# Kernel tuning notes

Measured on AMD Instinct MI355X. Metric: run time of the kernel, lower is better.

Reference implementation:

```python
import jax, jax.numpy as jnp
import numpy as np

B, T, F = 4096, 256, 20
VOCAB, EMB = 1281, 4
UNITS = (64, 32, 32, 32)


def setup_inputs() -> dict:
    key = jax.random.key(0)
    ks = jax.random.split(key, 16)
    feats = jax.random.normal(ks[0], (B, T, F), jnp.float32)
    ids = jax.random.randint(ks[1], (B, T), 0, VOCAB).astype(jnp.float32)
    input_tensor = feats.at[:, :, 1].set(ids)  # column 1 = org ids
    W_emb = jax.random.normal(ks[2], (VOCAB, EMB), jnp.float32) * 0.1
    in_dims = (F - 2 + 1 + EMB,) + UNITS[:-1]  # (23, 64, 32, 32)
    out = {"input_tensor": input_tensor, "W_emb": W_emb}
    for i, (din, u) in enumerate(zip(in_dims, UNITS)):
        out[f"k{i}"] = jax.random.normal(ks[3 + 3 * i], (din, 3 * u), jnp.float32) * 0.1
        out[f"rk{i}"] = jax.random.normal(ks[4 + 3 * i], (u, 3 * u), jnp.float32) * 0.1
        out[f"b{i}"] = jnp.zeros((2, 3 * u), jnp.float32)  # [input_bias, recurrent_bias] (reset_after)
    out["Wd"] = jax.random.normal(ks[15], (UNITS[-1], 2), jnp.float32) * 0.1
    out["bd"] = jnp.zeros((2,), jnp.float32)
    return out


def _gru(h, x, k, rk, b):
    # Keras GRUCell, reset_after=True (TF2 default)
    mx = x @ k + b[0]
    mh = h @ rk + b[1]
    xz, xr, xh = jnp.split(mx, 3, axis=-1)
    hz, hr, hh = jnp.split(mh, 3, axis=-1)
    z = jax.nn.sigmoid(xz + hz)
    r = jax.nn.sigmoid(xr + hr)
    hc = jnp.tanh(xh + r * hh)
    return z * h + (1.0 - z) * hc


def reference(input_tensor, W_emb, k0, rk0, b0, k1, rk1, b1, k2, rk2, b2, k3, rk3, b3, Wd, bd):
    f0 = input_tensor[:, :, :1]                      # [B,T,1]
    ids = input_tensor[:, :, 1].astype(jnp.int32)    # [B,T]
    rest = input_tensor[:, :, 2:]                    # [B,T,F-2]
    emb = W_emb[ids]                                 # [B,T,EMB]
    x = jnp.concatenate([f0, rest, emb], axis=-1)    # [B,T,F+3]
    xs = jnp.swapaxes(x, 0, 1)                       # [T,B,F+3]
    bsz = x.shape[0]
    h_init = tuple(jnp.zeros((bsz, u), x.dtype) for u in UNITS)
    layer_params = ((k0, rk0, b0), (k1, rk1, b1), (k2, rk2, b2), (k3, rk3, b3))

    def step(carry, xt):
        hs = []
        inp = xt
        for h, (k, rk, b) in zip(carry, layer_params):
            h = _gru(h, inp, k, rk, b)
            hs.append(h)
            inp = h
        return tuple(hs), None

    hs, _ = jax.lax.scan(step, h_init, xs)
    # return_sequences + [:, -1, :] == final hidden state of last layer
    logits = hs[-1] @ Wd + bd
    return jax.nn.softmax(logits, axis=-1)
```

## Files before the change

### kernel.cpp

```cpp
#include <hip/hip_runtime.h>


typedef __attribute__((ext_vector_type(8))) __bf16 bf16x8;
typedef __attribute__((ext_vector_type(4))) float f32x4;

#define TT 256
#define FF 20
#define BT 16
#define CH 64
#define SH0 72
#define SH1 40
#define XSTR 648
#define NTHR 768

__device__ __forceinline__ f32x4 mfma16(bf16x8 a, bf16x8 b, f32x4 c) {
  return __builtin_amdgcn_mfma_f32_16x16x32_bf16(a, b, c, 0, 0, 0);
}

__device__ __forceinline__ float sigm(float x) {
  return __builtin_amdgcn_rcpf(1.f + __builtin_amdgcn_exp2f(-1.44269504f * x));
}
__device__ __forceinline__ float tanh_(float x) {
  return __builtin_amdgcn_rcpf(1.f + __builtin_amdgcn_exp2f(-2.88539008f * x)) * 2.f - 1.f;
}

__device__ __forceinline__ bf16x8 bfragW(const float* W, int Kreal, int N,
                                         int ncol, int kbase) {
  bf16x8 r;
#pragma unroll
  for (int j = 0; j < 8; ++j) {
    int k = kbase + j;
    r[j] = (__bf16)(k < Kreal ? W[k * N + ncol] : 0.f);
  }
  return r;
}

extern "C" __global__ void __launch_bounds__(NTHR, 3)
gru4(const float* __restrict__ inp, const float* __restrict__ Wemb,
     const float* __restrict__ k0, const float* __restrict__ rk0, const float* __restrict__ b0,
     const float* __restrict__ k1, const float* __restrict__ rk1, const float* __restrict__ b1,
     const float* __restrict__ k2, const float* __restrict__ rk2, const float* __restrict__ b2,
     const float* __restrict__ k3, const float* __restrict__ rk3, const float* __restrict__ b3,
     const float* __restrict__ Wd, const float* __restrict__ bd,
     float* __restrict__ out)
{
  __shared__ __align__(16) __bf16 x_ch[CH * XSTR];
  __shared__ __align__(16) __bf16 h0_lds[2][BT * SH0];
  __shared__ __align__(16) __bf16 h1_lds[2][BT * SH1];
  __shared__ __align__(16) __bf16 h2_lds[2][BT * SH1];
  __shared__ __align__(16) __bf16 h3_lds[2][BT * SH1];
  __shared__ __align__(16) float h3f[BT * 32];

  const int tid  = threadIdx.x;
  const int lane = tid & 63;
  const int w    = tid >> 6;
  const int col  = lane & 15;
  const int kb   = (lane >> 4) * 8;
  const int rowq = (lane >> 4) * 4;
  const long bbase = (long)blockIdx.x * BT;
  const float* binp = inp + bbase * TT * FF;

  bf16x8 zf;
#pragma unroll
  for (int j = 0; j < 8; ++j) zf[j] = (__bf16)0.f;

  bf16x8 Wz0 = zf, Wz1 = zf, Wz2 = zf;
  bf16x8 Wr0 = zf, Wr1 = zf, Wr2 = zf;
  bf16x8 Wgx0 = zf, Wgx1 = zf, Wgx2 = zf;
  bf16x8 Wgh0 = zf, Wgh1 = zf, Wgh2 = zf;
  float bz = 0.f, br = 0.f, bxh = 0.f, bhh = 0.f;
  const __bf16 *A0b = x_ch, *A1b = x_ch, *A2b = x_ch;
  int D0 = 0, D1 = 0, D2 = 0;
  __bf16* Wwr0 = (__bf16*)h3f;
  int WD = 0, wstride = SH1;
  int lay = 0;
  bool doLo = false, doHi = false, threeA = false;

  if (w < 6) {
    lay = 0; threeA = true;
    const int sl = (w < 4) ? (w >> 1) : (w - 2);
    doLo = (w >= 4) || ((w & 1) == 0);
    doHi = (w >= 4) || ((w & 1) == 1);
    const int u = sl * 16 + col;
    Wz0 = bfragW(k0, 23, 192, u, kb);
    Wz1 = bfragW(rk0, 64, 192, u, kb);
    Wz2 = bfragW(rk0, 64, 192, u, 32 + kb);
    Wr0 = bfragW(k0, 23, 192, 64 + u, kb);
    Wr1 = bfragW(rk0, 64, 192, 64 + u, kb);
    Wr2 = bfragW(rk0, 64, 192, 64 + u, 32 + kb);
    Wgx0 = bfragW(k0, 23, 192, 128 + u, kb);
    Wgh1 = bfragW(rk0, 64, 192, 128 + u, kb);
    Wgh2 = bfragW(rk0, 64, 192, 128 + u, 32 + kb);
    bz  = b0[u] + b0[192 + u];
    br  = b0[64 + u] + b0[192 + 64 + u];
    bxh = b0[128 + u];
    bhh = b0[192 + 128 + u];
    A1b = &h0_lds[0][col * SH0 + kb];      D1 = BT * SH0;
    A2b = &h0_lds[0][col * SH0 + 32 + kb]; D2 = BT * SH0;
    Wwr0 = &h0_lds[0][rowq * SH0 + sl * 16 + col];
    WD = BT * SH0; wstride = SH0;
  } else if (w < 8) {
    lay = 1; threeA = true; doLo = doHi = true;
    const int u = (w - 6) * 16 + col;
    Wz0 = bfragW(k1, 64, 96, u, kb);
    Wz1 = bfragW(k1, 64, 96, u, 32 + kb);
    Wz2 = bfragW(rk1, 32, 96, u, kb);
    Wr0 = bfragW(k1, 64, 96, 32 + u, kb);
    Wr1 = bfragW(k1, 64, 96, 32 + u, 32 + kb);
    Wr2 = bfragW(rk1, 32, 96, 32 + u, kb);
    Wgx0 = bfragW(k1, 64, 96, 64 + u, kb);
    Wgx1 = bfragW(k1, 64, 96, 64 + u, 32 + kb);
    Wgh2 = bfragW(rk1, 32, 96, 64 + u, kb);
    bz  = b1[u] + b1[96 + u];
    br  = b1[32 + u] + b1[96 + 32 + u];
    bxh = b1[64 + u];
    bhh = b1[96 + 64 + u];
    A0b = &h0_lds[0][col * SH0 + kb];      D0 = BT * SH0;
    A1b = &h0_lds[0][col * SH0 + 32 + kb]; D1 = BT * SH0;
    A2b = &h1_lds[0][col * SH1 + kb];      D2 = BT * SH1;
    Wwr0 = &h1_lds[0][rowq * SH1 + (w - 6) * 16 + col];
    WD = BT * SH1; wstride = SH1;
  } else if (w < 10) {
    lay = 2; threeA = false; doLo = doHi = true;
    const int u = (w - 8) * 16 + col;
    Wz0 = bfragW(k2, 32, 96, u, kb);
    Wz1 = bfragW(rk2, 32, 96, u, kb);
    Wr0 = bfragW(k2, 32, 96, 32 + u, kb);
    Wr1 = bfragW(rk2, 32, 96, 32 + u, kb);
    Wgx0 = bfragW(k2, 32, 96, 64 + u, kb);
    Wgh1 = bfragW(rk2, 32, 96, 64 + u, kb);
    bz  = b2[u] + b2[96 + u];
    br  = b2[32 + u] + b2[96 + 32 + u];
    bxh = b2[64 + u];
    bhh = b2[96 + 64 + u];
    A0b = &h1_lds[0][col * SH1 + kb]; D0 = BT * SH1;
    A1b = &h2_lds[0][col * SH1 + kb]; D1 = BT * SH1;
    A2b = A1b; D2 = D1;
    Wwr0 = &h2_lds[0][rowq * SH1 + (w - 8) * 16 + col];
    WD = BT * SH1; wstride = SH1;
  } else {
    lay = 3; threeA = false; doLo = doHi = true;
    const int u = (w - 10) * 16 + col;
    Wz0 = bfragW(k3, 32, 96, u, kb);
    Wz1 = bfragW(rk3, 32, 96, u, kb);
    Wr0 = bfragW(k3, 32, 96, 32 + u, kb);
    Wr1 = bfragW(rk3, 32, 96, 32 + u, kb);
    Wgx0 = bfragW(k3, 32, 96, 64 + u, kb);
    Wgh1 = bfragW(rk3, 32, 96, 64 + u, kb);
    bz  = b3[u] + b3[96 + u];
    br  = b3[32 + u] + b3[96 + 32 + u];
    bxh = b3[64 + u];
    bhh = b3[96 + 64 + u];
    A0b = &h2_lds[0][col * SH1 + kb]; D0 = BT * SH1;
    A1b = &h3_lds[0][col * SH1 + kb]; D1 = BT * SH1;
    A2b = A1b; D2 = D1;
    Wwr0 = &h3_lds[0][rowq * SH1 + (w - 10) * 16 + col];
    WD = BT * SH1; wstride = SH1;
  }

  const __bf16* xb = &x_ch[col * 40 + kb];

  {
    __bf16* p0 = (__bf16*)h0_lds;
    for (int i = tid; i < 2 * BT * SH0; i += NTHR) p0[i] = (__bf16)0.f;
    __bf16* p1 = (__bf16*)h1_lds;
    __bf16* p2 = (__bf16*)h2_lds;
    __bf16* p3 = (__bf16*)h3_lds;
    for (int i = tid; i < 2 * BT * SH1; i += NTHR) {
      p1[i] = (__bf16)0.f; p2[i] = (__bf16)0.f; p3[i] = (__bf16)0.f;
    }
  }
  float hreg[4] = {0.f, 0.f, 0.f, 0.f};
  __syncthreads();

  for (int s = 0; s < TT + 3; ++s) {
    if ((s & (CH - 1)) == 0 && s < TT) {
      for (int idx = tid; idx < BT * CH; idx += NTHR) {
        const int row = idx >> 6;
        const int tg  = idx & (CH - 1);
        const float* p = binp + ((long)row * TT + s + tg) * FF;
        float4 v0 = *(const float4*)(p);
        float4 v1 = *(const float4*)(p + 4);
        float4 v2 = *(const float4*)(p + 8);
        float4 v3 = *(const float4*)(p + 12);
        float4 v4 = *(const float4*)(p + 16);
        float4 e  = *(const float4*)(Wemb + 4 * (int)v0.y);
        __bf16* d = &x_ch[tg * XSTR + row * 40];
        bf16x8 q0 = {(__bf16)v0.x, (__bf16)v0.z, (__bf16)v0.w, (__bf16)v1.x,
                     (__bf16)v1.y, (__bf16)v1.z, (__bf16)v1.w, (__bf16)v2.x};
        bf16x8 q1 = {(__bf16)v2.y, (__bf16)v2.z, (__bf16)v2.w, (__bf16)v3.x,
                     (__bf16)v3.y, (__bf16)v3.z, (__bf16)v3.w, (__bf16)v4.x};
        bf16x8 q2 = {(__bf16)v4.y, (__bf16)v4.z, (__bf16)v4.w, (__bf16)e.x,
                     (__bf16)e.y,  (__bf16)e.z,  (__bf16)e.w,  (__bf16)0.f};
        *(bf16x8*)(d)      = q0;
        *(bf16x8*)(d + 8)  = q1;
        *(bf16x8*)(d + 16) = q2;
        *(bf16x8*)(d + 24) = zf;
      }
      __syncthreads();
    }

    const int pb = (s + 1) & 1;
    const int qb = s & 1;
    const int t  = s - lay;

    if (t >= 0 && t < TT) {
      const __bf16* a0p = (lay == 0) ? (xb + (s & (CH - 1)) * XSTR)
                                     : (A0b + pb * D0);
      bf16x8 A0 = *(const bf16x8*)a0p;
      bf16x8 A1 = *(const bf16x8*)(A1b + pb * D1);
      f32x4 az  = {bz, bz, bz, bz};
      f32x4 ar  = {br, br, br, br};
      f32x4 axh = {bxh, bxh, bxh, bxh};
      f32x4 ahh = {bhh, bhh, bhh, bhh};
      az  = mfma16(A0, Wz0, az);   az  = mfma16(A1, Wz1, az);
      ar  = mfma16(A0, Wr0, ar);   ar  = mfma16(A1, Wr1, ar);
      axh = mfma16(A0, Wgx0, axh); axh = mfma16(A1, Wgx1, axh);
      ahh = mfma16(A0, Wgh0, ahh); ahh = mfma16(A1, Wgh1, ahh);
      if (threeA) {
        bf16x8 A2 = *(const bf16x8*)(A2b + pb * D2);
        az  = mfma16(A2, Wz2, az);
        ar  = mfma16(A2, Wr2, ar);
        axh = mfma16(A2, Wgx2, axh);
        ahh = mfma16(A2, Wgh2, ahh);
      }
      __bf16* wr = Wwr0 + qb * WD;

#define GATE(r) { \
        float z  = sigm(az[r]); \
        float rg = sigm(ar[r]); \
        float hc = tanh_(fmaf(rg, ahh[r], axh[r])); \
        float hn = fmaf(z, hreg[r] - hc, hc); \
        hreg[r] = hn; \
        wr[(r) * wstride] = (__bf16)hn; }

      if (doLo) { GATE(0); GATE(1); }
      if (doHi) { GATE(2); GATE(3); }
#undef GATE
    }

    __syncthreads();
  }

  if (w >= 10) {
#pragma unroll
    for (int r = 0; r < 4; ++r)
      h3f[(rowq + r) * 32 + (w - 10) * 16 + col] = hreg[r];
  }
  __syncthreads();

  if (tid < BT) {
    float l0 = bd[0], l1 = bd[1];
#pragma unroll
    for (int u = 0; u < 32; ++u) {
      float h = h3f[tid * 32 + u];
      l0 = fmaf(h, Wd[2 * u], l0);
      l1 = fmaf(h, Wd[2 * u + 1], l1);
    }
    float m = fmaxf(l0, l1);
    float e0 = __builtin_amdgcn_exp2f((l0 - m) * 1.44269504f);
    float e1 = __builtin_amdgcn_exp2f((l1 - m) * 1.44269504f);
    float inv = 1.f / (e0 + e1);
    out[(bbase + tid) * 2 + 0] = e0 * inv;
    out[(bbase + tid) * 2 + 1] = e1 * inv;
  }
}

extern "C" void kernel_launch(void* const* d_in, const int* in_sizes, int n_in,
                              void* d_out, int out_size, void* d_ws, size_t ws_size,
                              hipStream_t stream) {
  const float* inp  = (const float*)d_in[0];
  const float* Wemb = (const float*)d_in[1];
  const float* k0   = (const float*)d_in[2];
  const float* rk0  = (const float*)d_in[3];
  const float* b0   = (const float*)d_in[4];
  const float* k1   = (const float*)d_in[5];
  const float* rk1  = (const float*)d_in[6];
  const float* b1   = (const float*)d_in[7];
  const float* k2   = (const float*)d_in[8];
  const float* rk2  = (const float*)d_in[9];
  const float* b2   = (const float*)d_in[10];
  const float* k3   = (const float*)d_in[11];
  const float* rk3  = (const float*)d_in[12];
  const float* b3   = (const float*)d_in[13];
  const float* Wd   = (const float*)d_in[14];
  const float* bd   = (const float*)d_in[15];
  float* out = (float*)d_out;

  const int Btot = in_sizes[0] / (TT * FF);
  dim3 grid(Btot / BT);
  gru4<<<grid, NTHR, 0, stream>>>(inp, Wemb, k0, rk0, b0, k1, rk1, b1,
                                  k2, rk2, b2, k3, rk3, b3, Wd, bd, out);
}
```

Measured before the change: 342.9 us.

## Skew layers by two steps, prefetch layer inputs, and drop redundant gate MFMAs

```diff
diff --git a/kernel.cpp b/kernel.cpp
--- a/kernel.cpp
+++ b/kernel.cpp
@@ -12,16 +12,10 @@
 #define SH1 40
 #define XSTR 648
 #define NTHR 768
+#define LOG2E 1.44269504f
 
 __device__ __forceinline__ f32x4 mfma16(bf16x8 a, bf16x8 b, f32x4 c) {
   return __builtin_amdgcn_mfma_f32_16x16x32_bf16(a, b, c, 0, 0, 0);
-}
-
-__device__ __forceinline__ float sigm(float x) {
-  return __builtin_amdgcn_rcpf(1.f + __builtin_amdgcn_exp2f(-1.44269504f * x));
-}
-__device__ __forceinline__ float tanh_(float x) {
-  return __builtin_amdgcn_rcpf(1.f + __builtin_amdgcn_exp2f(-2.88539008f * x)) * 2.f - 1.f;
 }
 
 __device__ __forceinline__ bf16x8 bfragW(const float* W, int Kreal, int N,
@@ -64,96 +58,93 @@
 #pragma unroll
   for (int j = 0; j < 8; ++j) zf[j] = (__bf16)0.f;
 
-  bf16x8 Wz0 = zf, Wz1 = zf, Wz2 = zf;
-  bf16x8 Wr0 = zf, Wr1 = zf, Wr2 = zf;
-  bf16x8 Wgx0 = zf, Wgx1 = zf, Wgx2 = zf;
-  bf16x8 Wgh0 = zf, Wgh1 = zf, Wgh2 = zf;
+  bf16x8 WzP = zf, WrP = zf, WgP = zf;
+  bf16x8 WzX = zf, WrX = zf, WgX = zf;
+  bf16x8 WzO = zf, WrO = zf, WgO = zf;
   float bz = 0.f, br = 0.f, bxh = 0.f, bhh = 0.f;
-  const __bf16 *A0b = x_ch, *A1b = x_ch, *A2b = x_ch;
-  int D0 = 0, D1 = 0, D2 = 0;
+  const __bf16 *P0b = x_ch, *X1b = x_ch, *O0b = x_ch;
+  int DP = 0, DX = 0, DO = 0;
   __bf16* Wwr0 = (__bf16*)h3f;
   int WD = 0, wstride = SH1;
   int lay = 0;
-  bool doLo = false, doHi = false, threeA = false;
+  bool doLo = false, doHi = false, hasX1pre = false, hasX1own = false;
 
   if (w < 6) {
-    lay = 0; threeA = true;
+    lay = 0; hasX1own = true;
     const int sl = (w < 4) ? (w >> 1) : (w - 2);
     doLo = (w >= 4) || ((w & 1) == 0);
     doHi = (w >= 4) || ((w & 1) == 1);
     const int u = sl * 16 + col;
-    Wz0 = bfragW(k0, 23, 192, u, kb);
-    Wz1 = bfragW(rk0, 64, 192, u, kb);
-    Wz2 = bfragW(rk0, 64, 192, u, 32 + kb);
-    Wr0 = bfragW(k0, 23, 192, 64 + u, kb);
-    Wr1 = bfragW(rk0, 64, 192, 64 + u, kb);
-    Wr2 = bfragW(rk0, 64, 192, 64 + u, 32 + kb);
-    Wgx0 = bfragW(k0, 23, 192, 128 + u, kb);
-    Wgh1 = bfragW(rk0, 64, 192, 128 + u, kb);
-    Wgh2 = bfragW(rk0, 64, 192, 128 + u, 32 + kb);
+    WzP = bfragW(k0, 23, 192, u, kb);
+    WrP = bfragW(k0, 23, 192, 64 + u, kb);
+    WgP = bfragW(k0, 23, 192, 128 + u, kb);
+    WzO = bfragW(rk0, 64, 192, u, kb);
+    WrO = bfragW(rk0, 64, 192, 64 + u, kb);
+    WgO = bfragW(rk0, 64, 192, 128 + u, kb);
+    WzX = bfragW(rk0, 64, 192, u, 32 + kb);
+    WrX = bfragW(rk0, 64, 192, 64 + u, 32 + kb);
+    WgX = bfragW(rk0, 64, 192, 128 + u, 32 + kb);
     bz  = b0[u] + b0[192 + u];
     br  = b0[64 + u] + b0[192 + 64 + u];
     bxh = b0[128 + u];
     bhh = b0[192 + 128 + u];
-    A1b = &h0_lds[0][col * SH0 + kb];      D1 = BT * SH0;
-    A2b = &h0_lds[0][col * SH0 + 32 + kb]; D2 = BT * SH0;
+    O0b = &h0_lds[0][col * SH0 + kb];      DO = BT * SH0;
+    X1b = &h0_lds[0][col * SH0 + 32 + kb]; DX = BT * SH0;
     Wwr0 = &h0_lds[0][rowq * SH0 + sl * 16 + col];
     WD = BT * SH0; wstride = SH0;
   } else if (w < 8) {
-    lay = 1; threeA = true; doLo = doHi = true;
+    lay = 1; hasX1pre = true; doLo = doHi = true;
     const int u = (w - 6) * 16 + col;
-    Wz0 = bfragW(k1, 64, 96, u, kb);
-    Wz1 = bfragW(k1, 64, 96, u, 32 + kb);
-    Wz2 = bfragW(rk1, 32, 96, u, kb);
-    Wr0 = bfragW(k1, 64, 96, 32 + u, kb);
-    Wr1 = bfragW(k1, 64, 96, 32 + u, 32 + kb);
-    Wr2 = bfragW(rk1, 32, 96, 32 + u, kb);
-    Wgx0 = bfragW(k1, 64, 96, 64 + u, kb);
-    Wgx1 = bfragW(k1, 64, 96, 64 + u, 32 + kb);
-    Wgh2 = bfragW(rk1, 32, 96, 64 + u, kb);
+    WzP = bfragW(k1, 64, 96, u, kb);
+    WrP = bfragW(k1, 64, 96, 32 + u, kb);
+    WgP = bfragW(k1, 64, 96, 64 + u, kb);
+    WzX = bfragW(k1, 64, 96, u, 32 + kb);
+    WrX = bfragW(k1, 64, 96, 32 + u, 32 + kb);
+    WgX = bfragW(k1, 64, 96, 64 + u, 32 + kb);
+    WzO = bfragW(rk1, 32, 96, u, kb);
+    WrO = bfragW(rk1, 32, 96, 32 + u, kb);
+    WgO = bfragW(rk1, 32, 96, 64 + u, kb);
     bz  = b1[u] + b1[96 + u];
     br  = b1[32 + u] + b1[96 + 32 + u];
     bxh = b1[64 + u];
     bhh = b1[96 + 64 + u];
-    A0b = &h0_lds[0][col * SH0 + kb];      D0 = BT * SH0;
-    A1b = &h0_lds[0][col * SH0 + 32 + kb]; D1 = BT * SH0;
-    A2b = &h1_lds[0][col * SH1 + kb];      D2 = BT * SH1;
+    P0b = &h0_lds[0][col * SH0 + kb];      DP = BT * SH0;
+    X1b = &h0_lds[0][col * SH0 + 32 + kb]; DX = BT * SH0;
+    O0b = &h1_lds[0][col * SH1 + kb];      DO = BT * SH1;
     Wwr0 = &h1_lds[0][rowq * SH1 + (w - 6) * 16 + col];
     WD = BT * SH1; wstride = SH1;
   } else if (w < 10) {
-    lay = 2; threeA = false; doLo = doHi = true;
+    lay = 2; doLo = doHi = true;
     const int u = (w - 8) * 16 + col;
-    Wz0 = bfragW(k2, 32, 96, u, kb);
-    Wz1 = bfragW(rk2, 32, 96, u, kb);
-    Wr0 = bfragW(k2, 32, 96, 32 + u, kb);
-    Wr1 = bfragW(rk2, 32, 96, 32 + u, kb);
-    Wgx0 = bfragW(k2, 32, 96, 64 + u, kb);
-    Wgh1 = bfragW(rk2, 32, 96, 64 + u, kb);
+    WzP = bfragW(k2, 32, 96, u, kb);
+    WrP = bfragW(k2, 32, 96, 32 + u, kb);
+    WgP = bfragW(k2, 32, 96, 64 + u, kb);
+    WzO = bfragW(rk2, 32, 96, u, kb);
+    WrO = bfragW(rk2, 32, 96, 32 + u, kb);
+    WgO = bfragW(rk2, 32, 96, 64 + u, kb);
     bz  = b2[u] + b2[96 + u];
     br  = b2[32 + u] + b2[96 + 32 + u];
     bxh = b2[64 + u];
     bhh = b2[96 + 64 + u];
-    A0b = &h1_lds[0][col * SH1 + kb]; D0 = BT * SH1;
-    A1b = &h2_lds[0][col * SH1 + kb]; D1 = BT * SH1;
-    A2b = A1b; D2 = D1;
+    P0b = &h1_lds[0][col * SH1 + kb]; DP = BT * SH1;
+    O0b = &h2_lds[0][col * SH1 + kb]; DO = BT * SH1;
     Wwr0 = &h2_lds[0][rowq * SH1 + (w - 8) * 16 + col];
     WD = BT * SH1; wstride = SH1;
   } else {
-    lay = 3; threeA = false; doLo = doHi = true;
+    lay = 3; doLo = doHi = true;
     const int u = (w - 10) * 16 + col;
-    Wz0 = bfragW(k3, 32, 96, u, kb);
-    Wz1 = bfragW(rk3, 32, 96, u, kb);
-    Wr0 = bfragW(k3, 32, 96, 32 + u, kb);
-    Wr1 = bfragW(rk3, 32, 96, 32 + u, kb);
-    Wgx0 = bfragW(k3, 32, 96, 64 + u, kb);
-    Wgh1 = bfragW(rk3, 32, 96, 64 + u, kb);
+    WzP = bfragW(k3, 32, 96, u, kb);
+    WrP = bfragW(k3, 32, 96, 32 + u, kb);
+    WgP = bfragW(k3, 32, 96, 64 + u, kb);
+    WzO = bfragW(rk3, 32, 96, u, kb);
+    WrO = bfragW(rk3, 32, 96, 32 + u, kb);
+    WgO = bfragW(rk3, 32, 96, 64 + u, kb);
     bz  = b3[u] + b3[96 + u];
     br  = b3[32 + u] + b3[96 + 32 + u];
     bxh = b3[64 + u];
     bhh = b3[96 + 64 + u];
-    A0b = &h2_lds[0][col * SH1 + kb]; D0 = BT * SH1;
-    A1b = &h3_lds[0][col * SH1 + kb]; D1 = BT * SH1;
-    A2b = A1b; D2 = D1;
+    P0b = &h2_lds[0][col * SH1 + kb]; DP = BT * SH1;
+    O0b = &h3_lds[0][col * SH1 + kb]; DO = BT * SH1;
     Wwr0 = &h3_lds[0][rowq * SH1 + (w - 10) * 16 + col];
     WD = BT * SH1; wstride = SH1;
   }
@@ -171,9 +162,10 @@
     }
   }
   float hreg[4] = {0.f, 0.f, 0.f, 0.f};
+  bf16x8 P0 = zf, X1 = zf;
   __syncthreads();
 
-  for (int s = 0; s < TT + 3; ++s) {
+  for (int s = 0; s < TT + 6; ++s) {
     if ((s & (CH - 1)) == 0 && s < TT) {
       for (int idx = tid; idx < BT * CH; idx += NTHR) {
         const int row = idx >> 6;
@@ -198,38 +190,66 @@
         *(bf16x8*)(d + 24) = zf;
       }
       __syncthreads();
+      if (lay == 0) P0 = *(const bf16x8*)(xb);
     }
 
     const int pb = (s + 1) & 1;
     const int qb = s & 1;
-    const int t  = s - lay;
-
-    if (t >= 0 && t < TT) {
-      const __bf16* a0p = (lay == 0) ? (xb + (s & (CH - 1)) * XSTR)
-                                     : (A0b + pb * D0);
-      bf16x8 A0 = *(const bf16x8*)a0p;
-      bf16x8 A1 = *(const bf16x8*)(A1b + pb * D1);
-      f32x4 az  = {bz, bz, bz, bz};
-      f32x4 ar  = {br, br, br, br};
-      f32x4 axh = {bxh, bxh, bxh, bxh};
-      f32x4 ahh = {bhh, bhh, bhh, bhh};
-      az  = mfma16(A0, Wz0, az);   az  = mfma16(A1, Wz1, az);
-      ar  = mfma16(A0, Wr0, ar);   ar  = mfma16(A1, Wr1, ar);
-      axh = mfma16(A0, Wgx0, axh); axh = mfma16(A1, Wgx1, axh);
-      ahh = mfma16(A0, Wgh0, ahh); ahh = mfma16(A1, Wgh1, ahh);
-      if (threeA) {
-        bf16x8 A2 = *(const bf16x8*)(A2b + pb * D2);
-        az  = mfma16(A2, Wz2, az);
-        ar  = mfma16(A2, Wr2, ar);
-        axh = mfma16(A2, Wgx2, axh);
-        ahh = mfma16(A2, Wgh2, ahh);
+    const int t  = s - 2 * lay;
+    const bool active = (t >= 0) && (t < TT);
+
+    f32x4 az, ar, axh, ahh;
+    bf16x8 O0;
+    if (active) {
+      O0 = *(const bf16x8*)(O0b + pb * DO);
+      if (hasX1own) X1 = *(const bf16x8*)(X1b + pb * DX);
+      az  = f32x4{bz, bz, bz, bz};
+      ar  = f32x4{br, br, br, br};
+      axh = f32x4{bxh, bxh, bxh, bxh};
+      ahh = f32x4{bhh, bhh, bhh, bhh};
+      az  = mfma16(P0, WzP, az);
+      ar  = mfma16(P0, WrP, ar);
+      axh = mfma16(P0, WgP, axh);
+      if (hasX1pre) {
+        az  = mfma16(X1, WzX, az);
+        ar  = mfma16(X1, WrX, ar);
+        axh = mfma16(X1, WgX, axh);
       }
+      az  = mfma16(O0, WzO, az);
+      ar  = mfma16(O0, WrO, ar);
+      ahh = mfma16(O0, WgO, ahh);
+      if (hasX1own) {
+        az  = mfma16(X1, WzX, az);
+        ar  = mfma16(X1, WrX, ar);
+        ahh = mfma16(X1, WgX, ahh);
+      }
+    }
+
+    const int tn = t + 1;
+    if (tn >= 0 && tn < TT) {
+      if (lay == 0) {
+        const int pl = (s + 1) & (CH - 1);
+        if (pl != 0) P0 = *(const bf16x8*)(xb + pl * XSTR);
+      } else {
+        P0 = *(const bf16x8*)(P0b + pb * DP);
+        if (hasX1pre) X1 = *(const bf16x8*)(X1b + pb * DX);
+      }
+    }
+
+    if (active) {
       __bf16* wr = Wwr0 + qb * WD;
-
 #define GATE(r) { \
-        float z  = sigm(az[r]); \
-        float rg = sigm(ar[r]); \
-        float hc = tanh_(fmaf(rg, ahh[r], axh[r])); \
+        float yz = fminf(fmaxf(az[r], -44.f), 44.f) * -LOG2E; \
+        float yr = fminf(fmaxf(ar[r], -44.f), 44.f) * -LOG2E; \
+        float Ez = __builtin_amdgcn_exp2f(yz); \
+        float Er = __builtin_amdgcn_exp2f(yr); \
+        float dz = 1.f + Ez, dr = 1.f + Er; \
+        float inv = __builtin_amdgcn_rcpf(dz * dr); \
+        float z  = inv * dr; \
+        float rg = inv * dz; \
+        float uu = fmaf(rg, ahh[r], axh[r]); \
+        float Eg = __builtin_amdgcn_exp2f(uu * (-2.f * LOG2E)); \
+        float hc = fmaf(2.f, __builtin_amdgcn_rcpf(1.f + Eg), -1.f); \
         float hn = fmaf(z, hreg[r] - hc, hc); \
         hreg[r] = hn; \
         wr[(r) * wstride] = (__bf16)hn; }
@@ -258,8 +278,8 @@
       l1 = fmaf(h, Wd[2 * u + 1], l1);
     }
     float m = fmaxf(l0, l1);
-    float e0 = __builtin_amdgcn_exp2f((l0 - m) * 1.44269504f);
-    float e1 = __builtin_amdgcn_exp2f((l1 - m) * 1.44269504f);
+    float e0 = __builtin_amdgcn_exp2f((l0 - m) * LOG2E);
+    float e1 = __builtin_amdgcn_exp2f((l1 - m) * LOG2E);
     float inv = 1.f / (e0 + e1);
     out[(bbase + tid) * 2 + 0] = e0 * inv;
     out[(bbase + tid) * 2 + 1] = e1 * inv;
```

Result: slower. 367.8 us (+7.3%).
